# Kernel tuning notes

Measured on AMD Instinct MI355X. Metric: run time of the kernel, lower is better.

The kernel has to match this reference:

```python
import jax, jax.numpy as jnp
import numpy as np


def setup_inputs() -> dict:
    key = jax.random.key(0)
    k1, k2 = jax.random.split(key)
    x = jax.random.normal(k1, (2, 8, 32, 32, 64), dtype=jnp.float32)
    gamma = jax.random.normal(k2, (1,), dtype=jnp.float32)
    return {"x": x, "gamma": gamma}


def reference(x, gamma):
    # x: (B, D, H, W, C) -> flatten spatial dims to N = D*H*W
    B, D, H, W, C = x.shape
    N = D * H * W
    q = x.reshape(B, N, C)                       # proj_query (B, N, C)
    # energy = Q @ Q^T : (B, N, N) self-similarity over spatial positions
    energy = jnp.einsum('bnc,bmc->bnm', q, q)
    attn = jax.nn.softmax(energy, axis=-1)       # softmax over last axis (keras default)
    out = jnp.einsum('bnm,bmc->bnc', attn, q)    # attention @ Q -> (B, N, C)
    out = out.reshape(B, D, H, W, C)
    return gamma * out + x
```

## Files before the change

### kernel.cpp

```cpp
#include <hip/hip_runtime.h>
#include <hip/hip_bf16.h>

typedef __attribute__((ext_vector_type(8))) short bf16x8;
typedef __attribute__((ext_vector_type(16))) float f32x16;
typedef __attribute__((ext_vector_type(4))) int int4v;

#define NB 2
#define NN 8192
#define NC 64
#define LOG2E 1.44269504088896340736f
#define MAXNORM_BOUND 16.0f
#define KSTRIDE 68
#define SKIP_THRESH -110.0f

union I4 { int4v v; unsigned long long u[2]; };

__device__ __forceinline__ bf16x8 lds_ld16(const __hip_bfloat16* p) {
    union { bf16x8 v; unsigned long long u[2]; } r;
    r.u[0] = *(const unsigned long long*)(p);
    r.u[1] = *(const unsigned long long*)(p + 4);
    return r.v;
}
__device__ __forceinline__ bf16x8 lds_ld2x8(const __hip_bfloat16* p) {
    union { bf16x8 v; unsigned long long u[2]; } r;
    r.u[0] = *(const unsigned long long*)(p);
    r.u[1] = *(const unsigned long long*)(p + 8);
    return r.v;
}

__global__ __launch_bounds__(256) void prep_kernel(
        const float* __restrict__ x,
        __hip_bfloat16* __restrict__ qb,
        __hip_bfloat16* __restrict__ qt) {
    __shared__ __align__(16) __hip_bfloat16 T[64][72];
    const int blk = blockIdx.x;
    const int b  = blk >> 7;
    const int n0 = (blk & 127) << 6;
    const int tid = threadIdx.x;

#pragma unroll
    for (int v = 0; v < 2; ++v) {
        const int vid = tid + (v << 8);
        const int row = vid >> 3;
        const int cb  = (vid & 7) << 3;
        const float* src = x + (((size_t)(b * NN + n0 + row)) << 6) + cb;
        float4 f0 = *(const float4*)(src);
        float4 f1 = *(const float4*)(src + 4);
        __align__(16) __hip_bfloat16 h[8];
        h[0] = __float2bfloat16(f0.x); h[1] = __float2bfloat16(f0.y);
        h[2] = __float2bfloat16(f0.z); h[3] = __float2bfloat16(f0.w);
        h[4] = __float2bfloat16(f1.x); h[5] = __float2bfloat16(f1.y);
        h[6] = __float2bfloat16(f1.z); h[7] = __float2bfloat16(f1.w);
        *(int4v*)(qb + (((size_t)(b * NN + n0 + row)) << 6) + cb) = *(const int4v*)h;
        *(int4v*)(&T[row][cb]) = *(const int4v*)h;
    }
    __syncthreads();
#pragma unroll
    for (int v = 0; v < 2; ++v) {
        const int vid = tid + (v << 8);
        const int c  = vid >> 3;
        const int nb = (vid & 7) << 3;
        __align__(16) __hip_bfloat16 h[8];
#pragma unroll
        for (int j = 0; j < 8; ++j) h[j] = T[nb + j][c];
        *(int4v*)(qt + (((size_t)(b * NC + c)) << 13) + n0 + nb) = *(const int4v*)h;
    }
}

template <int LSPLIT>
__global__ __launch_bounds__(256, 4) void attn_kernel(
        const __hip_bfloat16* __restrict__ qb,
        const __hip_bfloat16* __restrict__ qt,
        float* __restrict__ opart,
        float* __restrict__ lpart) {
    constexpr int SPLIT = 1 << LSPLIT;
    constexpr int KT_PER = 128 / SPLIT;

    __shared__ __hip_bfloat16 KVs[2][64][KSTRIDE];
    __shared__ __hip_bfloat16 KVt[2][64][KSTRIDE];

    const int blk   = blockIdx.x;
    const int chunk = blk & (SPLIT - 1);
    const int qt_i  = (blk >> LSPLIT) & 63;
    const int b     = blk >> (6 + LSPLIT);
    const int q0    = qt_i << 7;
    const int tid  = threadIdx.x;
    const int wave = tid >> 6;
    const int lane = tid & 63;
    const int n5   = lane & 31;
    const int h    = lane >> 5;

    const __hip_bfloat16* kvptr = qb + ((size_t)b << 19);
    const __hip_bfloat16* ktptr = qt + ((size_t)b << 19);

    const int srow = tid >> 3;
    const int scb  = (tid & 7) << 3;

    const __hip_bfloat16* qrow = kvptr + (((size_t)(q0 + (wave << 5) + n5)) << 6);
    bf16x8 Qf[4];
#pragma unroll
    for (int step = 0; step < 4; ++step)
        Qf[step] = *(const bf16x8*)(qrow + (step << 4) + (h << 3));

    float mb2;
    {
        float s = 0.f;
#pragma unroll
        for (int step = 0; step < 4; ++step)
#pragma unroll
            for (int j = 0; j < 8; ++j) {
                float f = __uint_as_float(((unsigned)(unsigned short)Qf[step][j]) << 16);
                s += f * f;
            }
        s += __shfl_xor(s, 32);
        mb2 = sqrtf(s) * (MAXNORM_BOUND * LOG2E);
    }

    f32x16 O0 = (f32x16)(0.f), O1 = (f32x16)(0.f);
    float lp = 0.f;

    const int kt0 = chunk * KT_PER;

    {
        const int kb = kt0 << 6;
#pragma unroll
        for (int v = 0; v < 2; ++v) {
            const int row = srow + (v << 5);
            I4 gs, gt;
            gs.v = *(const int4v*)(kvptr + (((size_t)(kb + row)) << 6) + scb);
            gt.v = *(const int4v*)(ktptr + (((size_t)row) << 13) + kb + scb);
            *(unsigned long long*)(&KVs[0][row][scb])     = gs.u[0];
            *(unsigned long long*)(&KVs[0][row][scb + 4]) = gs.u[1];
            *(unsigned long long*)(&KVt[0][row][scb])     = gt.u[0];
            *(unsigned long long*)(&KVt[0][row][scb + 4]) = gt.u[1];
        }
    }

    int cur = 0;
    for (int i = 0; i < KT_PER; ++i) {
        __syncthreads();

        I4 gs0, gs1, gt0, gt1;
        const bool more = (i + 1 < KT_PER);
        if (more) {
            const int kb = (kt0 + i + 1) << 6;
            gs0.v = *(const int4v*)(kvptr + (((size_t)(kb + srow)) << 6) + scb);
            gt0.v = *(const int4v*)(ktptr + (((size_t)srow) << 13) + kb + scb);
            gs1.v = *(const int4v*)(kvptr + (((size_t)(kb + srow + 32)) << 6) + scb);
            gt1.v = *(const int4v*)(ktptr + (((size_t)(srow + 32)) << 13) + kb + scb);
        }

        f32x16 ST0 = (f32x16)(0.f), ST1 = (f32x16)(0.f);
#pragma unroll
        for (int step = 0; step < 4; ++step) {
            bf16x8 a0 = lds_ld16(&KVs[cur][n5][(step << 4) + (h << 3)]);
            bf16x8 a1 = lds_ld16(&KVs[cur][32 + n5][(step << 4) + (h << 3)]);
            ST0 = __builtin_amdgcn_mfma_f32_32x32x16_bf16(a0, Qf[step], ST0, 0, 0, 0);
            ST1 = __builtin_amdgcn_mfma_f32_32x32x16_bf16(a1, Qf[step], ST1, 0, 0, 0);
        }

        float mx = ST0[0];
#pragma unroll
        for (int r = 1; r < 16; ++r) mx = fmaxf(mx, ST0[r]);
#pragma unroll
        for (int r = 0; r < 16; ++r) mx = fmaxf(mx, ST1[r]);
        const bool keep = fmaf(mx, LOG2E, -mb2) >= SKIP_THRESH;

        if (__ballot(keep) != 0ull) {
            bf16x8 bP[4];
#pragma unroll
            for (int s = 0; s < 4; ++s) {
#pragma unroll
                for (int j = 0; j < 8; ++j) {
                    const float sv = (s < 2) ? ST0[((s & 1) << 3) + j] : ST1[((s & 1) << 3) + j];
                    float p = __builtin_amdgcn_exp2f(fmaf(sv, LOG2E, -mb2));
                    lp += p;
                    bP[s][j] = __builtin_bit_cast(short, __float2bfloat16(p));
                }
            }

#pragma unroll
            for (int s = 0; s < 4; ++s) {
                bf16x8 a0 = lds_ld2x8(&KVt[cur][n5][(s << 4) + (h << 2)]);
                bf16x8 a1 = lds_ld2x8(&KVt[cur][32 + n5][(s << 4) + (h << 2)]);
                O0 = __builtin_amdgcn_mfma_f32_32x32x16_bf16(a0, bP[s], O0, 0, 0, 0);
                O1 = __builtin_amdgcn_mfma_f32_32x32x16_bf16(a1, bP[s], O1, 0, 0, 0);
            }
        }

        if (more) {
            const int nb_ = cur ^ 1;
            *(unsigned long long*)(&KVs[nb_][srow][scb])          = gs0.u[0];
            *(unsigned long long*)(&KVs[nb_][srow][scb + 4])      = gs0.u[1];
            *(unsigned long long*)(&KVt[nb_][srow][scb])          = gt0.u[0];
            *(unsigned long long*)(&KVt[nb_][srow][scb + 4])      = gt0.u[1];
            *(unsigned long long*)(&KVs[nb_][srow + 32][scb])     = gs1.u[0];
            *(unsigned long long*)(&KVs[nb_][srow + 32][scb + 4]) = gs1.u[1];
            *(unsigned long long*)(&KVt[nb_][srow + 32][scb])     = gt1.u[0];
            *(unsigned long long*)(&KVt[nb_][srow + 32][scb + 4]) = gt1.u[1];
        }
        cur ^= 1;
    }

    float lsum = lp;
    lsum += __shfl_xor(lsum, 32);
    if (h == 0)
        lpart[(chunk << 14) + (b << 13) + q0 + (wave << 5) + n5] = lsum;

    float* orow = opart + ((size_t)chunk << 20) +
                  (((size_t)(b * NN + q0 + (wave << 5) + n5)) << 6);
#pragma unroll
    for (int g4 = 0; g4 < 4; ++g4) {
        float4 f0 = make_float4(O0[(g4 << 2)], O0[(g4 << 2) + 1],
                                O0[(g4 << 2) + 2], O0[(g4 << 2) + 3]);
        *(float4*)(orow + (g4 << 3) + (h << 2)) = f0;
        float4 f1 = make_float4(O1[(g4 << 2)], O1[(g4 << 2) + 1],
                                O1[(g4 << 2) + 2], O1[(g4 << 2) + 3]);
        *(float4*)(orow + 32 + (g4 << 3) + (h << 2)) = f1;
    }
}

template <int LSPLIT>
__global__ __launch_bounds__(256) void finalize_kernel(
        const float* __restrict__ x,
        const float* __restrict__ gamma_p,
        const float* __restrict__ opart,
        const float* __restrict__ lpart,
        float* __restrict__ out) {
    constexpr int SPLIT = 1 << LSPLIT;
    const int i4 = blockIdx.x * 256 + threadIdx.x;
    const size_t e = (size_t)i4 << 2;
    const int rowg = i4 >> 4;

    float l = 0.f;
#pragma unroll
    for (int c = 0; c < SPLIT; ++c) l += lpart[(c << 14) + rowg];

    float4 o = make_float4(0.f, 0.f, 0.f, 0.f);
#pragma unroll
    for (int c = 0; c < SPLIT; ++c) {
        float4 t = *(const float4*)(opart + ((size_t)c << 20) + e);
        o.x += t.x; o.y += t.y; o.z += t.z; o.w += t.w;
    }
    const float inv = 1.0f / l;
    const float gm = gamma_p[0];
    float4 xin = *(const float4*)(x + e);
    float4 r;
    r.x = gm * (o.x * inv) + xin.x;
    r.y = gm * (o.y * inv) + xin.y;
    r.z = gm * (o.z * inv) + xin.z;
    r.w = gm * (o.w * inv) + xin.w;
    *(float4*)(out + e) = r;
}

extern "C" void kernel_launch(void* const* d_in, const int* in_sizes, int n_in,
                              void* d_out, int out_size, void* d_ws, size_t ws_size,
                              hipStream_t stream) {
    const float* x     = (const float*)d_in[0];
    const float* gamma = (const float*)d_in[1];
    float* out = (float*)d_out;

    __hip_bfloat16* qb = (__hip_bfloat16*)d_ws;
    __hip_bfloat16* qt = qb + (size_t)NB * NN * NC;
    float* opart = (float*)((char*)d_ws + (size_t)4 * 1024 * 1024 + 256);

    prep_kernel<<<256, 256, 0, stream>>>(x, qb, qt);

    const size_t base = (size_t)4 * 1024 * 1024 + 256;
    const size_t need8 = base + ((size_t)8 * NB * NN * NC + (size_t)8 * NB * NN) * 4;
    if (ws_size >= need8) {
        float* lpart = opart + (size_t)8 * NB * NN * NC;
        attn_kernel<3><<<NB * 64 * 8, 256, 0, stream>>>(qb, qt, opart, lpart);
        finalize_kernel<3><<<(NB * NN * NC / 4) / 256, 256, 0, stream>>>(x, gamma, opart, lpart, out);
    } else {
        float* lpart = opart + (size_t)4 * NB * NN * NC;
        attn_kernel<2><<<NB * 64 * 4, 256, 0, stream>>>(qb, qt, opart, lpart);
        finalize_kernel<2><<<(NB * NN * NC / 4) / 256, 256, 0, stream>>>(x, gamma, opart, lpart, out);
    }
}
```

Before: 93.66 us.

## Load V operand directly from global only for kept tiles; skip empty partial writes

Measured after the change: 103.4 us. +10.4%, slower.

```diff
diff --git a/kernel.cpp b/kernel.cpp
--- a/kernel.cpp
+++ b/kernel.cpp
@@ -21,7 +21,7 @@
     r.u[1] = *(const unsigned long long*)(p + 4);
     return r.v;
 }
-__device__ __forceinline__ bf16x8 lds_ld2x8(const __hip_bfloat16* p) {
+__device__ __forceinline__ bf16x8 ld2x8(const __hip_bfloat16* p) {
     union { bf16x8 v; unsigned long long u[2]; } r;
     r.u[0] = *(const unsigned long long*)(p);
     r.u[1] = *(const unsigned long long*)(p + 8);
@@ -77,7 +77,6 @@
     constexpr int KT_PER = 128 / SPLIT;
 
     __shared__ __hip_bfloat16 KVs[2][64][KSTRIDE];
-    __shared__ __hip_bfloat16 KVt[2][64][KSTRIDE];
 
     const int blk   = blockIdx.x;
     const int chunk = blk & (SPLIT - 1);
@@ -118,6 +117,7 @@
 
     f32x16 O0 = (f32x16)(0.f), O1 = (f32x16)(0.f);
     float lp = 0.f;
+    bool wkeep = false;
 
     const int kt0 = chunk * KT_PER;
 
@@ -126,13 +126,10 @@
 #pragma unroll
         for (int v = 0; v < 2; ++v) {
             const int row = srow + (v << 5);
-            I4 gs, gt;
+            I4 gs;
             gs.v = *(const int4v*)(kvptr + (((size_t)(kb + row)) << 6) + scb);
-            gt.v = *(const int4v*)(ktptr + (((size_t)row) << 13) + kb + scb);
             *(unsigned long long*)(&KVs[0][row][scb])     = gs.u[0];
             *(unsigned long long*)(&KVs[0][row][scb + 4]) = gs.u[1];
-            *(unsigned long long*)(&KVt[0][row][scb])     = gt.u[0];
-            *(unsigned long long*)(&KVt[0][row][scb + 4]) = gt.u[1];
         }
     }
 
@@ -140,14 +137,12 @@
     for (int i = 0; i < KT_PER; ++i) {
         __syncthreads();
 
-        I4 gs0, gs1, gt0, gt1;
+        I4 gs0, gs1;
         const bool more = (i + 1 < KT_PER);
         if (more) {
             const int kb = (kt0 + i + 1) << 6;
             gs0.v = *(const int4v*)(kvptr + (((size_t)(kb + srow)) << 6) + scb);
-            gt0.v = *(const int4v*)(ktptr + (((size_t)srow) << 13) + kb + scb);
             gs1.v = *(const int4v*)(kvptr + (((size_t)(kb + srow + 32)) << 6) + scb);
-            gt1.v = *(const int4v*)(ktptr + (((size_t)(srow + 32)) << 13) + kb + scb);
         }
 
         f32x16 ST0 = (f32x16)(0.f), ST1 = (f32x16)(0.f);
@@ -167,6 +162,18 @@
         const bool keep = fmaf(mx, LOG2E, -mb2) >= SKIP_THRESH;
 
         if (__ballot(keep) != 0ull) {
+            wkeep = true;
+            const int kb = (kt0 + i) << 6;
+
+            const __hip_bfloat16* v0 = ktptr + ((size_t)n5 << 13)        + kb + (h << 2);
+            const __hip_bfloat16* v1 = ktptr + ((size_t)(32 + n5) << 13) + kb + (h << 2);
+            bf16x8 vA0[4], vA1[4];
+#pragma unroll
+            for (int s = 0; s < 4; ++s) {
+                vA0[s] = ld2x8(v0 + (s << 4));
+                vA1[s] = ld2x8(v1 + (s << 4));
+            }
+
             bf16x8 bP[4];
 #pragma unroll
             for (int s = 0; s < 4; ++s) {
@@ -181,10 +188,8 @@
 
 #pragma unroll
             for (int s = 0; s < 4; ++s) {
-                bf16x8 a0 = lds_ld2x8(&KVt[cur][n5][(s << 4) + (h << 2)]);
-                bf16x8 a1 = lds_ld2x8(&KVt[cur][32 + n5][(s << 4) + (h << 2)]);
-                O0 = __builtin_amdgcn_mfma_f32_32x32x16_bf16(a0, bP[s], O0, 0, 0, 0);
-                O1 = __builtin_amdgcn_mfma_f32_32x32x16_bf16(a1, bP[s], O1, 0, 0, 0);
+                O0 = __builtin_amdgcn_mfma_f32_32x32x16_bf16(vA0[s], bP[s], O0, 0, 0, 0);
+                O1 = __builtin_amdgcn_mfma_f32_32x32x16_bf16(vA1[s], bP[s], O1, 0, 0, 0);
             }
         }
 
@@ -192,12 +197,8 @@
             const int nb_ = cur ^ 1;
             *(unsigned long long*)(&KVs[nb_][srow][scb])          = gs0.u[0];
             *(unsigned long long*)(&KVs[nb_][srow][scb + 4])      = gs0.u[1];
-            *(unsigned long long*)(&KVt[nb_][srow][scb])          = gt0.u[0];
-            *(unsigned long long*)(&KVt[nb_][srow][scb + 4])      = gt0.u[1];
             *(unsigned long long*)(&KVs[nb_][srow + 32][scb])     = gs1.u[0];
             *(unsigned long long*)(&KVs[nb_][srow + 32][scb + 4]) = gs1.u[1];
-            *(unsigned long long*)(&KVt[nb_][srow + 32][scb])     = gt1.u[0];
-            *(unsigned long long*)(&KVt[nb_][srow + 32][scb + 4]) = gt1.u[1];
         }
         cur ^= 1;
     }
@@ -207,16 +208,18 @@
     if (h == 0)
         lpart[(chunk << 14) + (b << 13) + q0 + (wave << 5) + n5] = lsum;
 
-    float* orow = opart + ((size_t)chunk << 20) +
-                  (((size_t)(b * NN + q0 + (wave << 5) + n5)) << 6);
-#pragma unroll
-    for (int g4 = 0; g4 < 4; ++g4) {
-        float4 f0 = make_float4(O0[(g4 << 2)], O0[(g4 << 2) + 1],
-                                O0[(g4 << 2) + 2], O0[(g4 << 2) + 3]);
-        *(float4*)(orow + (g4 << 3) + (h << 2)) = f0;
-        float4 f1 = make_float4(O1[(g4 << 2)], O1[(g4 << 2) + 1],
-                                O1[(g4 << 2) + 2], O1[(g4 << 2) + 3]);
-        *(float4*)(orow + 32 + (g4 << 3) + (h << 2)) = f1;
+    if (wkeep) {
+        float* orow = opart + ((size_t)chunk << 20) +
+                      (((size_t)(b * NN + q0 + (wave << 5) + n5)) << 6);
+#pragma unroll
+        for (int g4 = 0; g4 < 4; ++g4) {
+            float4 f0 = make_float4(O0[(g4 << 2)], O0[(g4 << 2) + 1],
+                                    O0[(g4 << 2) + 2], O0[(g4 << 2) + 3]);
+            *(float4*)(orow + (g4 << 3) + (h << 2)) = f0;
+            float4 f1 = make_float4(O1[(g4 << 2)], O1[(g4 << 2) + 1],
+                                    O1[(g4 << 2) + 2], O1[(g4 << 2) + 3]);
+            *(float4*)(orow + 32 + (g4 << 3) + (h << 2)) = f1;
+        }
     }
 }
 
@@ -233,14 +236,15 @@
     const int rowg = i4 >> 4;
 
     float l = 0.f;
-#pragma unroll
-    for (int c = 0; c < SPLIT; ++c) l += lpart[(c << 14) + rowg];
-
     float4 o = make_float4(0.f, 0.f, 0.f, 0.f);
 #pragma unroll
     for (int c = 0; c < SPLIT; ++c) {
-        float4 t = *(const float4*)(opart + ((size_t)c << 20) + e);
-        o.x += t.x; o.y += t.y; o.z += t.z; o.w += t.w;
+        const float lc = lpart[(c << 14) + rowg];
+        l += lc;
+        if (lc != 0.f) {
+            float4 t = *(const float4*)(opart + ((size_t)c << 20) + e);
+            o.x += t.x; o.y += t.y; o.z += t.z; o.w += t.w;
+        }
     }
     const float inv = 1.0f / l;
     const float gm = gamma_p[0];
```
